# Kernel tuning notes

Measured on AMD Instinct MI355X. Metric: run time of the kernel, lower is better.

## Reference

```python
import jax, jax.numpy as jnp
import numpy as np


def _apply_ry(state, theta, i, n):
    # state: [B, 2^n] complex; theta: scalar or [B]
    B = state.shape[0]
    s = state.reshape(B, 2**i, 2, 2**(n - i - 1))
    th = jnp.reshape(theta, (-1, 1, 1)) * 0.5
    c, sn = jnp.cos(th), jnp.sin(th)
    a0, a1 = s[:, :, 0], s[:, :, 1]
    return jnp.stack([c * a0 - sn * a1, sn * a0 + c * a1], axis=2).reshape(B, -1)


def _apply_rz(state, theta, i, n):
    B = state.shape[0]
    s = state.reshape(B, 2**i, 2, 2**(n - i - 1))
    ph = jnp.exp(-0.5j * jnp.reshape(theta, (-1, 1, 1)).astype(jnp.float32))
    return jnp.stack([s[:, :, 0] * ph, s[:, :, 1] * jnp.conj(ph)], axis=2).reshape(B, -1)


def _apply_cnot(state, c, t, n):
    # CNOT(control=c, target=t); flips target amplitudes on control=1 slice
    B = state.shape[0]
    s = state.reshape((B,) + (2,) * n)
    ax_c, ax_t = 1 + c, 1 + t
    zero = jnp.take(s, 0, axis=ax_c)
    one = jnp.take(s, 1, axis=ax_c)
    one = jnp.flip(one, axis=ax_t - (1 if t > c else 0))
    return jnp.stack([zero, one], axis=ax_c).reshape(B, -1)


def _z_signs(n):
    # signs[i, k] = +1 if bit i of basis index k is 0 else -1 (qubit 0 = MSB)
    idx = np.arange(2**n)
    bits = (idx[None, :] >> (n - 1 - np.arange(n))[:, None]) & 1
    return jnp.asarray(1.0 - 2.0 * bits, dtype=jnp.float32)  # [n, 2^n]


def _circuit(q_in, w_ry, w_rz):
    # Batched state-vector simulation of: AngleEmbedding(RY) ->
    # n_layers x (per-qubit RY,RZ + CNOT ring) -> <Z_i> expectations.
    B, n = q_in.shape
    L = w_ry.shape[0]
    state = jnp.zeros((B, 2**n), jnp.complex64).at[:, 0].set(1.0)
    for i in range(n):  # AngleEmbedding with rotation='Y'
        state = _apply_ry(state, q_in[:, i], i, n)
    for l in range(L):
        for i in range(n):
            state = _apply_ry(state, w_ry[l, i], i, n)
            state = _apply_rz(state, w_rz[l, i], i, n)
        for i in range(n):  # CNOT ring
            state = _apply_cnot(state, i, (i + 1) % n, n)
    probs = jnp.abs(state) ** 2  # [B, 2^n]
    return probs @ _z_signs(n).T  # [B, n] = <Z_i>


def setup_inputs():
    key = jax.random.key(0)
    ks = jax.random.split(key, 6)
    B, D, n, L = 4096, 512, 10, 4
    return {
        "x": jax.random.normal(ks[0], (B, D), jnp.float32),
        "pre_w": jax.random.normal(ks[1], (n, D), jnp.float32) / np.sqrt(D).astype(np.float32),
        "pre_b": jnp.zeros((n,), jnp.float32),
        "post_w": jax.random.normal(ks[2], (1, n), jnp.float32) / np.sqrt(n).astype(np.float32),
        "post_b": jnp.zeros((1,), jnp.float32),
        "w_ry": jax.random.normal(ks[3], (L, n), jnp.float32),
        "w_rz": jax.random.normal(ks[4], (L, n), jnp.float32),
    }


def reference(x, pre_w, pre_b, post_w, post_b, w_ry, w_rz):
    q_in = x @ pre_w.T + pre_b      # pre_net: [B, n_qubits] rotation angles
    z = _circuit(q_in, w_ry, w_rz)  # [B, n_qubits] PauliZ expectations
    return z @ post_w.T + post_b    # post_net: [B, 1] logits
```

## Files before the change

kernel.cpp:

```cpp
#include <hip/hip_runtime.h>

#define DEV static __device__ __forceinline__

template <int CTRL>
DEV float dpp_xor(float v) {
    int i = __float_as_int(v);
    i = __builtin_amdgcn_update_dpp(i, i, CTRL, 0xF, 0xF, false);
    return __int_as_float(i);
}
template <int PAT>
DEV float swz(float v) {
    return __int_as_float(__builtin_amdgcn_ds_swizzle(__float_as_int(v), PAT));
}
DEV float bperm(int byteaddr, float v) {
    return __int_as_float(__builtin_amdgcn_ds_bpermute(byteaddr, __float_as_int(v)));
}

template <int MASK>
DEV float lanexor(float v, int a32) {
    if constexpr (MASK == 1)       return dpp_xor<0xB1>(v);
    else if constexpr (MASK == 2)  return dpp_xor<0x4E>(v);
    else if constexpr (MASK == 8)  return dpp_xor<0x128>(v);
    else if constexpr (MASK == 4)  return swz<0x101F>(v);
    else if constexpr (MASK == 16) return swz<0x401F>(v);
    else                           return bperm(a32, v);
}

DEV float wave_sum(float v, int a32) {
    v += lanexor<1>(v, 0);
    v += lanexor<2>(v, 0);
    v += lanexor<4>(v, 0);
    v += lanexor<8>(v, 0);
    v += lanexor<16>(v, 0);
    v += bperm(a32, v);
    return v;
}


template <int P>
DEV void apply_ry(float (&re)[16], float (&im)[16], float c, float s, int lane, int a32) {
    if constexpr (P >= 4) {
        constexpr int mask = 1 << (P - 4);
        const float sg = (lane & mask) ? s : -s;
#pragma unroll
        for (int r = 0; r < 16; ++r) {
            float pr = lanexor<mask>(re[r], a32);
            float pi = lanexor<mask>(im[r], a32);
            re[r] = fmaf(c, re[r], sg * pr);
            im[r] = fmaf(c, im[r], sg * pi);
        }
    } else {
        constexpr int tb = 1 << P;
#pragma unroll
        for (int r = 0; r < 16; ++r) {
            if (!(r & tb)) {
                const int r2 = r | tb;
                float a0r = re[r], a1r = re[r2];
                float a0i = im[r], a1i = im[r2];
                re[r]  = fmaf(c, a0r, -s * a1r);
                re[r2] = fmaf(s, a0r,  c * a1r);
                im[r]  = fmaf(c, a0i, -s * a1i);
                im[r2] = fmaf(s, a0i,  c * a1i);
            }
        }
    }
}

DEV int g_of(int a) {
    a ^= ((a >> 1) & 1) ? 1 : 0;
    a ^= ((a >> 2) & 1) ? 2 : 0;
    a ^= ((a >> 3) & 1) ? 4 : 0;
    a ^= ((a >> 4) & 1) ? 8 : 0;
    a ^= ((a >> 5) & 1) ? 16 : 0;
    return a;
}

__global__ void dqc_trig_kernel(const float* __restrict__ w_ry,
                                const float* __restrict__ w_rz,
                                float2* __restrict__ trig) {
    int t = threadIdx.x;
    if (t < 80) {
        float ang = (t < 40 ? w_ry[t] : w_rz[t - 40]) * 0.5f;
        trig[t] = make_float2(__cosf(ang), __sinf(ang));
    }
}

__global__ __launch_bounds__(256, 4) void dqc_main_kernel(
    const float* __restrict__ x, const float* __restrict__ pre_w,
    const float* __restrict__ pre_b, const float* __restrict__ post_w,
    const float* __restrict__ post_b, const float2* __restrict__ trig,
    float* __restrict__ out, int B) {
    const int lane = threadIdx.x & 63;
    const int wid = threadIdx.x >> 6;
    const int b = blockIdx.x * 4 + wid;
    if (b >= B) return;

    const int a32 = (lane ^ 32) << 2;
    const int h0 = lane ^ ((lane & 1) ? 32 : 0);
    const int cA = g_of(h0) << 2;
    const int cB = g_of(h0 ^ 32) << 2;

    float th[10];
#pragma unroll
    for (int i = 0; i < 10; ++i) th[i] = 0.f;
    const float* xb = x + (size_t)b * 512;
#pragma unroll
    for (int k = 0; k < 8; ++k) {
        const int idx = lane + 64 * k;
        float xv = xb[idx];
#pragma unroll
        for (int i = 0; i < 10; ++i) th[i] = fmaf(xv, pre_w[i * 512 + idx], th[i]);
    }
#pragma unroll
    for (int i = 0; i < 10; ++i) th[i] = wave_sum(th[i], a32) + pre_b[i];

    float cc[10], ss[10];
#pragma unroll
    for (int i = 0; i < 10; ++i) {
        float a = th[i] * 0.5f;
        cc[i] = __cosf(a);
        ss[i] = __sinf(a);
    }
    float laneP = 1.f;
#pragma unroll
    for (int i = 0; i < 6; ++i)
        laneP *= ((lane >> (5 - i)) & 1) ? ss[i] : cc[i];
    float hi4[4], lo4[4];
#pragma unroll
    for (int j = 0; j < 4; ++j) {
        float f6 = (j >> 1) ? ss[6] : cc[6];
        float f7 = (j & 1) ? ss[7] : cc[7];
        hi4[j] = laneP * f6 * f7;
        float f8 = (j >> 1) ? ss[8] : cc[8];
        float f9 = (j & 1) ? ss[9] : cc[9];
        lo4[j] = f8 * f9;
    }
    float re[16], im[16];
#pragma unroll
    for (int r = 0; r < 16; ++r) { re[r] = hi4[r >> 2] * lo4[r & 3]; im[r] = 0.f; }

#pragma unroll 1
    for (int l = 0; l < 4; ++l) {
        const float2* tr = trig + l * 10;
        const float2* tz = trig + 40 + l * 10;

        apply_ry<9>(re, im, tr[0].x, tr[0].y, lane, a32);
        apply_ry<8>(re, im, tr[1].x, tr[1].y, lane, a32);
        apply_ry<7>(re, im, tr[2].x, tr[2].y, lane, a32);
        apply_ry<6>(re, im, tr[3].x, tr[3].y, lane, a32);
        apply_ry<5>(re, im, tr[4].x, tr[4].y, lane, a32);
        apply_ry<4>(re, im, tr[5].x, tr[5].y, lane, a32);
        apply_ry<3>(re, im, tr[6].x, tr[6].y, lane, a32);
        apply_ry<2>(re, im, tr[7].x, tr[7].y, lane, a32);
        apply_ry<1>(re, im, tr[8].x, tr[8].y, lane, a32);
        apply_ry<0>(re, im, tr[9].x, tr[9].y, lane, a32);

        float plr, pli;
        {
            float2 z0 = tz[0];
            pli = ((lane >> 5) & 1) ? z0.y : -z0.y;
            plr = z0.x;
#pragma unroll
            for (int q = 1; q < 6; ++q) {
                float2 z = tz[q];
                float sq = ((lane >> (5 - q)) & 1) ? z.y : -z.y;
                float nr = plr * z.x - pli * sq;
                float ni = plr * sq + pli * z.x;
                plr = nr; pli = ni;
            }
        }
        float p67r[4], p67i[4], p89r[4], p89i[4];
        {
            const float c6 = tz[6].x, s6 = tz[6].y, c7 = tz[7].x, s7 = tz[7].y;
            const float c8 = tz[8].x, s8 = tz[8].y, c9 = tz[9].x, s9 = tz[9].y;
#pragma unroll
            for (int j = 0; j < 4; ++j) {
                float sg6 = (j >> 1) ? s6 : -s6;
                float sg7 = (j & 1) ? s7 : -s7;
                float ar = c6 * c7 - sg6 * sg7;
                float ai = c6 * sg7 + sg6 * c7;
                p67r[j] = ar * plr - ai * pli;
                p67i[j] = ar * pli + ai * plr;
                float sg8 = (j >> 1) ? s8 : -s8;
                float sg9 = (j & 1) ? s9 : -s9;
                p89r[j] = c8 * c9 - sg8 * sg9;
                p89i[j] = c8 * sg9 + sg8 * c9;
            }
        }
#pragma unroll
        for (int r = 0; r < 16; ++r) {
            const int j = r >> 2, k = r & 3;
            float t_r = re[r] * p67r[j] - im[r] * p67i[j];
            float t_i = re[r] * p67i[j] + im[r] * p67r[j];
            re[r] = t_r * p89r[k] - t_i * p89i[k];
            im[r] = t_r * p89i[k] + t_i * p89r[k];
        }

#pragma unroll
        for (int r = 0; r < 16; ++r) {
            const int addr = ((0x6996 >> r) & 1) ? cB : cA;
            re[r] = bperm(addr, re[r]);
            im[r] = bperm(addr, im[r]);
        }
        {
            const bool ctrl = (lane & 1) != 0;
#pragma unroll
            for (int r = 0; r < 8; ++r) {
                const int r2 = r | 8;
                float t0 = re[r], t1 = re[r2];
                re[r]  = ctrl ? t1 : t0;
                re[r2] = ctrl ? t0 : t1;
                float u0 = im[r], u1 = im[r2];
                im[r]  = ctrl ? u1 : u0;
                im[r2] = ctrl ? u0 : u1;
            }
        }
#pragma unroll
        for (int r = 0; r < 16; ++r)
            if ((r & 8) && !(r & 4)) {
                const int r2 = r | 4;
                float t = re[r]; re[r] = re[r2]; re[r2] = t;
                t = im[r]; im[r] = im[r2]; im[r2] = t;
            }
#pragma unroll
        for (int r = 0; r < 16; ++r)
            if ((r & 4) && !(r & 2)) {
                const int r2 = r | 2;
                float t = re[r]; re[r] = re[r2]; re[r2] = t;
                t = im[r]; im[r] = im[r2]; im[r2] = t;
            }
#pragma unroll
        for (int r = 0; r < 16; ++r)
            if ((r & 2) && !(r & 1)) {
                const int r2 = r | 1;
                float t = re[r]; re[r] = re[r2]; re[r2] = t;
                t = im[r]; im[r] = im[r2]; im[r2] = t;
            }
    }

    float laneC = 0.f;
#pragma unroll
    for (int j = 0; j < 6; ++j) {
        int bit = (lane >> (5 - j)) & 1;
        laneC += post_w[j] * (1.f - 2.f * (float)bit);
    }
    float acc = 0.f;
#pragma unroll
    for (int r = 0; r < 16; ++r) {
        float regC = 0.f;
#pragma unroll
        for (int j = 6; j < 10; ++j) {
            int bit = (r >> (9 - j)) & 1;
            regC += post_w[j] * (1.f - 2.f * (float)bit);
        }
        float p = fmaf(re[r], re[r], im[r] * im[r]);
        acc = fmaf(p, laneC + regC, acc);
    }
    acc = wave_sum(acc, a32);
    if (lane == 0) out[b] = acc + post_b[0];
}

extern "C" void kernel_launch(void* const* d_in, const int* in_sizes, int n_in,
                              void* d_out, int out_size, void* d_ws, size_t ws_size,
                              hipStream_t stream) {
    const float* x      = (const float*)d_in[0];
    const float* pre_w  = (const float*)d_in[1];
    const float* pre_b  = (const float*)d_in[2];
    const float* post_w = (const float*)d_in[3];
    const float* post_b = (const float*)d_in[4];
    const float* w_ry   = (const float*)d_in[5];
    const float* w_rz   = (const float*)d_in[6];
    float* out = (float*)d_out;
    float2* trig = (float2*)d_ws;

    const int B = in_sizes[0] / 512;

    dqc_trig_kernel<<<1, 128, 0, stream>>>(w_ry, w_rz, trig);
    dqc_main_kernel<<<(B + 3) / 4, 256, 0, stream>>>(x, pre_w, pre_b, post_w,
                                                     post_b, trig, out, B);
}
```

Baseline: 100.9 us.

## Fuse trig precompute into main kernel and use permlane swaps and DPP shuffles

Drops the separate trig kernel launch; each wave now computes the cos/sin of the RY/RZ weights inline. Cross-lane exchanges for the high qubits use the gfx950 permlane16/32 swap builtins when available, replacing ds_swizzle and ds_bpermute, and the xor-4 exchange becomes two DPP moves. The pre-net dot product switches to float4 vectorized loads. The cost is redundant trig work in every wave and a runtime check of the permlane lane convention.

```diff
diff --git a/kernel.cpp b/kernel.cpp
--- a/kernel.cpp
+++ b/kernel.cpp
@@ -3,7 +3,7 @@
 #define DEV static __device__ __forceinline__
 
 template <int CTRL>
-DEV float dpp_xor(float v) {
+DEV float dpp_mov(float v) {
     int i = __float_as_int(v);
     i = __builtin_amdgcn_update_dpp(i, i, CTRL, 0xF, 0xF, false);
     return __int_as_float(i);
@@ -16,36 +16,123 @@
     return __int_as_float(__builtin_amdgcn_ds_bpermute(byteaddr, __float_as_int(v)));
 }
 
-template <int MASK>
-DEV float lanexor(float v, int a32) {
-    if constexpr (MASK == 1)       return dpp_xor<0xB1>(v);
-    else if constexpr (MASK == 2)  return dpp_xor<0x4E>(v);
-    else if constexpr (MASK == 8)  return dpp_xor<0x128>(v);
-    else if constexpr (MASK == 4)  return swz<0x101F>(v);
-    else if constexpr (MASK == 16) return swz<0x401F>(v);
-    else                           return bperm(a32, v);
-}
+#if __has_builtin(__builtin_amdgcn_permlane16_swap)
+#define HAVE_PL16 1
+DEV void pl16_pair(float v, float &r0, float &r1) {
+    auto r = __builtin_amdgcn_permlane16_swap(__float_as_int(v), __float_as_int(v),
+                                              false, false);
+    r0 = __int_as_float((int)r[0]);
+    r1 = __int_as_float((int)r[1]);
+}
+#endif
+#if __has_builtin(__builtin_amdgcn_permlane32_swap)
+#define HAVE_PL32 1
+DEV void pl32_pair(float v, float &r0, float &r1) {
+    auto r = __builtin_amdgcn_permlane32_swap(__float_as_int(v), __float_as_int(v),
+                                              false, false);
+    r0 = __int_as_float((int)r[0]);
+    r1 = __int_as_float((int)r[1]);
+}
+#endif
 
 DEV float wave_sum(float v, int a32) {
-    v += lanexor<1>(v, 0);
-    v += lanexor<2>(v, 0);
-    v += lanexor<4>(v, 0);
-    v += lanexor<8>(v, 0);
-    v += lanexor<16>(v, 0);
+    v += dpp_mov<0xB1>(v);
+    v += dpp_mov<0x4E>(v);
+    v += dpp_mov<0x141>(v);
+    v += dpp_mov<0x128>(v);
+#ifdef HAVE_PL16
+    {
+        float r0, r1;
+        pl16_pair(v, r0, r1);
+        v = r0 + r1;
+    }
+#else
+    v += swz<0x401F>(v);
+#endif
+#ifdef HAVE_PL32
+    {
+        float r0, r1;
+        pl32_pair(v, r0, r1);
+        v = r0 + r1;
+    }
+#else
     v += bperm(a32, v);
+#endif
     return v;
 }
 
-
 template <int P>
-DEV void apply_ry(float (&re)[16], float (&im)[16], float c, float s, int lane, int a32) {
-    if constexpr (P >= 4) {
+DEV void apply_ry(float (&re)[16], float (&im)[16], float c, float s, int lane,
+                  int a32, bool cv16, bool cv32) {
+    if constexpr (P == 9) {
+#ifdef HAVE_PL32
+        const bool hi = (lane & 32) != 0;
+        const float fl = hi ? s : c;
+        const float fh = hi ? c : -s;
+        const float g0 = cv32 ? fl : fh;
+        const float g1 = cv32 ? fh : fl;
+#pragma unroll
+        for (int r = 0; r < 16; ++r) {
+            float x0, x1, y0, y1;
+            pl32_pair(re[r], x0, x1);
+            pl32_pair(im[r], y0, y1);
+            re[r] = fmaf(g0, x0, g1 * x1);
+            im[r] = fmaf(g0, y0, g1 * y1);
+        }
+#else
+        const float sg = (lane & 32) ? s : -s;
+#pragma unroll
+        for (int r = 0; r < 16; ++r) {
+            float pr = bperm(a32, re[r]);
+            float pi = bperm(a32, im[r]);
+            re[r] = fmaf(c, re[r], sg * pr);
+            im[r] = fmaf(c, im[r], sg * pi);
+        }
+#endif
+    } else if constexpr (P == 8) {
+#ifdef HAVE_PL16
+        const bool hi = (lane & 16) != 0;
+        const float fl = hi ? s : c;
+        const float fh = hi ? c : -s;
+        const float g0 = cv16 ? fl : fh;
+        const float g1 = cv16 ? fh : fl;
+#pragma unroll
+        for (int r = 0; r < 16; ++r) {
+            float x0, x1, y0, y1;
+            pl16_pair(re[r], x0, x1);
+            pl16_pair(im[r], y0, y1);
+            re[r] = fmaf(g0, x0, g1 * x1);
+            im[r] = fmaf(g0, y0, g1 * y1);
+        }
+#else
+        const float sg = (lane & 16) ? s : -s;
+#pragma unroll
+        for (int r = 0; r < 16; ++r) {
+            float pr = swz<0x401F>(re[r]);
+            float pi = swz<0x401F>(im[r]);
+            re[r] = fmaf(c, re[r], sg * pr);
+            im[r] = fmaf(c, im[r], sg * pi);
+        }
+#endif
+    } else if constexpr (P >= 4) {
         constexpr int mask = 1 << (P - 4);
         const float sg = (lane & mask) ? s : -s;
 #pragma unroll
         for (int r = 0; r < 16; ++r) {
-            float pr = lanexor<mask>(re[r], a32);
-            float pi = lanexor<mask>(im[r], a32);
+            float pr, pi;
+            if constexpr (mask == 8) {
+                pr = dpp_mov<0x128>(re[r]);
+                pi = dpp_mov<0x128>(im[r]);
+            } else if constexpr (mask == 4) {
+                pr = dpp_mov<0x1B>(dpp_mov<0x141>(re[r]));
+                pi = dpp_mov<0x1B>(dpp_mov<0x141>(im[r]));
+            } else if constexpr (mask == 2) {
+                pr = dpp_mov<0x4E>(re[r]);
+                pi = dpp_mov<0x4E>(im[r]);
+            } else {
+                pr = dpp_mov<0xB1>(re[r]);
+                pi = dpp_mov<0xB1>(im[r]);
+            }
             re[r] = fmaf(c, re[r], sg * pr);
             im[r] = fmaf(c, im[r], sg * pi);
         }
@@ -75,27 +162,32 @@
     return a;
 }
 
-__global__ void dqc_trig_kernel(const float* __restrict__ w_ry,
-                                const float* __restrict__ w_rz,
-                                float2* __restrict__ trig) {
-    int t = threadIdx.x;
-    if (t < 80) {
-        float ang = (t < 40 ? w_ry[t] : w_rz[t - 40]) * 0.5f;
-        trig[t] = make_float2(__cosf(ang), __sinf(ang));
-    }
-}
-
 __global__ __launch_bounds__(256, 4) void dqc_main_kernel(
     const float* __restrict__ x, const float* __restrict__ pre_w,
     const float* __restrict__ pre_b, const float* __restrict__ post_w,
-    const float* __restrict__ post_b, const float2* __restrict__ trig,
-    float* __restrict__ out, int B) {
+    const float* __restrict__ post_b, const float* __restrict__ w_ry,
+    const float* __restrict__ w_rz, float* __restrict__ out, int B) {
     const int lane = threadIdx.x & 63;
     const int wid = threadIdx.x >> 6;
     const int b = blockIdx.x * 4 + wid;
     if (b >= B) return;
 
     const int a32 = (lane ^ 32) << 2;
+
+    bool cv16 = false, cv32 = false;
+#ifdef HAVE_PL16
+    {
+        auto r = __builtin_amdgcn_permlane16_swap(lane, lane, false, false);
+        cv16 = ((int)r[0] == (lane & ~16));
+    }
+#endif
+#ifdef HAVE_PL32
+    {
+        auto r = __builtin_amdgcn_permlane32_swap(lane, lane, false, false);
+        cv32 = ((int)r[0] == (lane & ~32));
+    }
+#endif
+
     const int h0 = lane ^ ((lane & 1) ? 32 : 0);
     const int cA = g_of(h0) << 2;
     const int cB = g_of(h0 ^ 32) << 2;
@@ -103,13 +195,20 @@
     float th[10];
 #pragma unroll
     for (int i = 0; i < 10; ++i) th[i] = 0.f;
-    const float* xb = x + (size_t)b * 512;
-#pragma unroll
-    for (int k = 0; k < 8; ++k) {
+    const float4* xb4 = reinterpret_cast<const float4*>(x + (size_t)b * 512);
+    const float4* pw4 = reinterpret_cast<const float4*>(pre_w);
+#pragma unroll
+    for (int k = 0; k < 2; ++k) {
         const int idx = lane + 64 * k;
-        float xv = xb[idx];
-#pragma unroll
-        for (int i = 0; i < 10; ++i) th[i] = fmaf(xv, pre_w[i * 512 + idx], th[i]);
+        const float4 xv = xb4[idx];
+#pragma unroll
+        for (int i = 0; i < 10; ++i) {
+            const float4 wv = pw4[i * 128 + idx];
+            th[i] = fmaf(xv.x, wv.x, th[i]);
+            th[i] = fmaf(xv.y, wv.y, th[i]);
+            th[i] = fmaf(xv.z, wv.z, th[i]);
+            th[i] = fmaf(xv.w, wv.w, th[i]);
+        }
     }
 #pragma unroll
     for (int i = 0; i < 10; ++i) th[i] = wave_sum(th[i], a32) + pre_b[i];
@@ -141,38 +240,46 @@
 
 #pragma unroll 1
     for (int l = 0; l < 4; ++l) {
-        const float2* tr = trig + l * 10;
-        const float2* tz = trig + 40 + l * 10;
-
-        apply_ry<9>(re, im, tr[0].x, tr[0].y, lane, a32);
-        apply_ry<8>(re, im, tr[1].x, tr[1].y, lane, a32);
-        apply_ry<7>(re, im, tr[2].x, tr[2].y, lane, a32);
-        apply_ry<6>(re, im, tr[3].x, tr[3].y, lane, a32);
-        apply_ry<5>(re, im, tr[4].x, tr[4].y, lane, a32);
-        apply_ry<4>(re, im, tr[5].x, tr[5].y, lane, a32);
-        apply_ry<3>(re, im, tr[6].x, tr[6].y, lane, a32);
-        apply_ry<2>(re, im, tr[7].x, tr[7].y, lane, a32);
-        apply_ry<1>(re, im, tr[8].x, tr[8].y, lane, a32);
-        apply_ry<0>(re, im, tr[9].x, tr[9].y, lane, a32);
-
+        const float* wry = w_ry + l * 10;
+        const float* wrz = w_rz + l * 10;
+
+        {
+            float a;
+            a = wry[0] * 0.5f; apply_ry<9>(re, im, __cosf(a), __sinf(a), lane, a32, cv16, cv32);
+            a = wry[1] * 0.5f; apply_ry<8>(re, im, __cosf(a), __sinf(a), lane, a32, cv16, cv32);
+            a = wry[2] * 0.5f; apply_ry<7>(re, im, __cosf(a), __sinf(a), lane, a32, cv16, cv32);
+            a = wry[3] * 0.5f; apply_ry<6>(re, im, __cosf(a), __sinf(a), lane, a32, cv16, cv32);
+            a = wry[4] * 0.5f; apply_ry<5>(re, im, __cosf(a), __sinf(a), lane, a32, cv16, cv32);
+            a = wry[5] * 0.5f; apply_ry<4>(re, im, __cosf(a), __sinf(a), lane, a32, cv16, cv32);
+            a = wry[6] * 0.5f; apply_ry<3>(re, im, __cosf(a), __sinf(a), lane, a32, cv16, cv32);
+            a = wry[7] * 0.5f; apply_ry<2>(re, im, __cosf(a), __sinf(a), lane, a32, cv16, cv32);
+            a = wry[8] * 0.5f; apply_ry<1>(re, im, __cosf(a), __sinf(a), lane, a32, cv16, cv32);
+            a = wry[9] * 0.5f; apply_ry<0>(re, im, __cosf(a), __sinf(a), lane, a32, cv16, cv32);
+        }
+
+        float zc[10], zs[10];
+#pragma unroll
+        for (int q = 0; q < 10; ++q) {
+            float a = wrz[q] * 0.5f;
+            zc[q] = __cosf(a);
+            zs[q] = __sinf(a);
+        }
         float plr, pli;
         {
-            float2 z0 = tz[0];
-            pli = ((lane >> 5) & 1) ? z0.y : -z0.y;
-            plr = z0.x;
+            pli = ((lane >> 5) & 1) ? zs[0] : -zs[0];
+            plr = zc[0];
 #pragma unroll
             for (int q = 1; q < 6; ++q) {
-                float2 z = tz[q];
-                float sq = ((lane >> (5 - q)) & 1) ? z.y : -z.y;
-                float nr = plr * z.x - pli * sq;
-                float ni = plr * sq + pli * z.x;
+                float sq = ((lane >> (5 - q)) & 1) ? zs[q] : -zs[q];
+                float nr = plr * zc[q] - pli * sq;
+                float ni = plr * sq + pli * zc[q];
                 plr = nr; pli = ni;
             }
         }
         float p67r[4], p67i[4], p89r[4], p89i[4];
         {
-            const float c6 = tz[6].x, s6 = tz[6].y, c7 = tz[7].x, s7 = tz[7].y;
-            const float c8 = tz[8].x, s8 = tz[8].y, c9 = tz[9].x, s9 = tz[9].y;
+            const float c6 = zc[6], s6 = zs[6], c7 = zc[7], s7 = zs[7];
+            const float c8 = zc[8], s8 = zs[8], c9 = zc[9], s9 = zs[9];
 #pragma unroll
             for (int j = 0; j < 4; ++j) {
                 float sg6 = (j >> 1) ? s6 : -s6;
@@ -271,11 +378,10 @@
     const float* w_ry   = (const float*)d_in[5];
     const float* w_rz   = (const float*)d_in[6];
     float* out = (float*)d_out;
-    float2* trig = (float2*)d_ws;
+    (void)d_ws; (void)ws_size;
 
     const int B = in_sizes[0] / 512;
 
-    dqc_trig_kernel<<<1, 128, 0, stream>>>(w_ry, w_rz, trig);
     dqc_main_kernel<<<(B + 3) / 4, 256, 0, stream>>>(x, pre_w, pre_b, post_w,
-                                                     post_b, trig, out, B);
-}
+                                                     post_b, w_ry, w_rz, out, B);
+}
```

Result: slower. 106.5 us (+5.5%).
